# Kernel tuning notes

Measured on AMD Instinct MI355X. Metric: run time of the kernel, lower is better.

## Reference

```python
import jax, jax.numpy as jnp
import numpy as np

NEG_SLOPE = 0.2  # PyG GATConv default negative_slope
EPS = 1e-16      # PyG softmax denominator epsilon


def gat_conv(x, src, dst, W, b, att_src, att_dst, num_nodes):
    """PyG GATConv, heads=1, add_self_loops=True (self loops already in src/dst).
    x: [N, Fin]; src/dst: [E]; W: [Fin, Fout]; att_src/att_dst: [Fout]."""
    h = x @ W                                  # [N, Fout]
    a_src = h @ att_src                        # [N]
    a_dst = h @ att_dst                        # [N]
    e = jax.nn.leaky_relu(a_src[src] + a_dst[dst], NEG_SLOPE)  # [E]
    m = jax.ops.segment_max(e, dst, num_segments=num_nodes)    # softmax over edges grouped by dst
    ex = jnp.exp(e - m[dst])
    denom = jax.ops.segment_sum(ex, dst, num_segments=num_nodes)
    alpha = ex / (denom[dst] + EPS)            # [E]
    out = jax.ops.segment_sum(alpha[:, None] * h[src], dst, num_segments=num_nodes)
    return out + b


def global_attention(x, gate_w, gate_b):
    """PyG GlobalAttention with a single graph: softmax(gate_nn(x)) weighted sum."""
    gate = x @ gate_w + gate_b                 # [N, 1]
    attn = jax.nn.softmax(gate, axis=0)        # softmax over all nodes (one graph)
    return jnp.sum(attn * x, axis=0, keepdims=True)  # [1, F]


def setup_inputs() -> dict:
    key = jax.random.key(0)
    ks = jax.random.split(key, 12)
    N, E, D, H = 50000, 800000, 768, 256
    x = jax.random.normal(ks[0], (N, D), dtype=jnp.float32)
    edge_index = jax.random.randint(ks[1], (2, E), 0, N, dtype=jnp.int64)
    s = 1.0 / np.sqrt(D)
    W1 = jax.random.normal(ks[2], (D, H), dtype=jnp.float32) * s
    b1 = jnp.zeros((H,), dtype=jnp.float32)
    as1 = jax.random.normal(ks[3], (H,), dtype=jnp.float32) * (1.0 / np.sqrt(H))
    ad1 = jax.random.normal(ks[4], (H,), dtype=jnp.float32) * (1.0 / np.sqrt(H))
    s2 = 1.0 / np.sqrt(H)
    W2 = jax.random.normal(ks[5], (H, H), dtype=jnp.float32) * s2
    b2 = jnp.zeros((H,), dtype=jnp.float32)
    as2 = jax.random.normal(ks[6], (H,), dtype=jnp.float32) * s2
    ad2 = jax.random.normal(ks[7], (H,), dtype=jnp.float32) * s2
    gate_w = jax.random.normal(ks[8], (H, 1), dtype=jnp.float32) * s2
    gate_b = jnp.zeros((1,), dtype=jnp.float32)
    return {"x": x, "edge_index": edge_index, "W1": W1, "b1": b1, "as1": as1,
            "ad1": ad1, "W2": W2, "b2": b2, "as2": as2, "ad2": ad2,
            "gate_w": gate_w, "gate_b": gate_b}


def reference(x, edge_index, W1, b1, as1, ad1, W2, b2, as2, ad2, gate_w, gate_b):
    N = x.shape[0]
    loops = jnp.arange(N, dtype=edge_index.dtype)
    src = jnp.concatenate([edge_index[0], loops])  # add self loops (GATConv default)
    dst = jnp.concatenate([edge_index[1], loops])
    h = gat_conv(x, src, dst, W1, b1, as1, ad1, N)
    h = jax.nn.relu(h)
    h = gat_conv(h, src, dst, W2, b2, as2, ad2, N)
    h = jax.nn.relu(h)
    return global_attention(h, gate_w, gate_b)   # [1, 256]
```

## Files before the change

kernel.cpp:

```cpp
#include <hip/hip_runtime.h>

#define WAVE 64
#define LRELU(x) ((x) > 0.0f ? (x) : 0.2f * (x))
#define SB0 __builtin_amdgcn_sched_barrier(0)

typedef __attribute__((ext_vector_type(8))) short bf16x8;
typedef __attribute__((ext_vector_type(8))) unsigned short u16x8;
typedef __attribute__((ext_vector_type(4))) float f32x4;

__device__ __forceinline__ void gld16(const void* g, void* l) {
    __builtin_amdgcn_global_load_lds((const __attribute__((address_space(1))) unsigned int*)g,
                                     (__attribute__((address_space(3))) unsigned int*)l,
                                     16, 0, 0);
}

__device__ __forceinline__ unsigned short f2bf_hi(float f) {
    unsigned u = __builtin_bit_cast(unsigned, f);
    u += 0x7FFF + ((u >> 16) & 1);
    return (unsigned short)(u >> 16);
}

__device__ __forceinline__ void split8(f32x4 a, f32x4 b, bf16x8& hi, bf16x8& lo) {
    float f[8] = {a[0], a[1], a[2], a[3], b[0], b[1], b[2], b[3]};
#pragma unroll
    for (int e = 0; e < 8; e++) {
        unsigned u = __builtin_bit_cast(unsigned, f[e]);
        float hf = __builtin_bit_cast(float, u & 0xFFFF0000u);
        float fl = f[e] - hf;
        unsigned u2 = __builtin_bit_cast(unsigned, fl);
        unsigned t2 = u2 + 0x7FFF + ((u2 >> 16) & 1);
        hi[e] = (short)(u >> 16);
        lo[e] = (short)(t2 >> 16);
    }
}

__device__ __forceinline__ void split8t(f32x4 a, f32x4 b, bf16x8& hi, bf16x8& lo) {
    float f[8] = {a[0], a[1], a[2], a[3], b[0], b[1], b[2], b[3]};
#pragma unroll
    for (int e = 0; e < 8; e++) {
        unsigned u = __builtin_bit_cast(unsigned, f[e]);
        float hf = __builtin_bit_cast(float, u & 0xFFFF0000u);
        float fl = f[e] - hf;
        unsigned u2 = __builtin_bit_cast(unsigned, fl);
        hi[e] = (short)(u >> 16);
        lo[e] = (short)(u2 >> 16);
    }
}

__global__ __launch_bounds__(256) void k_gemm_f32A(const float* __restrict__ A,
                                                   const unsigned short* __restrict__ Bh,
                                                   unsigned short* __restrict__ Cb,
                                                   float* __restrict__ asrc,
                                                   float* __restrict__ adst,
                                                   const float* __restrict__ att_s,
                                                   const float* __restrict__ att_d,
                                                   int M, int K) {
    __shared__ char smem[65536];
    char* bA = smem;
    char* bB = smem + 49152;

    const int tid = threadIdx.x, lane = tid & 63, w = tid >> 6;
    const int m16 = lane & 15, q = lane >> 4;
    const int row0 = blockIdx.x * 128, col0 = blockIdx.y * 128;
    const int NT = K >> 5;

    f32x4 acc[4][4];
#pragma unroll
    for (int i = 0; i < 4; i++)
#pragma unroll
        for (int j = 0; j < 4; j++) acc[i][j] = (f32x4){0.f, 0.f, 0.f, 0.f};

    const float* apt[4];
    const int jA0 = w * 4;
#pragma unroll
    for (int jj = 0; jj < 4; jj++) {
        int j = jA0 + jj;
        int r = row0 + (j & 1) * 64 + lane;
        if (r > M - 1) r = M - 1;
        apt[jj] = A + (size_t)r * K + (j >> 1) * 4;
    }
    const unsigned short* bpt[2];
    const int jB0 = w * 2;
#pragma unroll
    for (int jj = 0; jj < 2; jj++) {
        int j = jB0 + jj;
        bpt[jj] = Bh + (size_t)(col0 + (j & 1) * 64 + lane) * K + (j >> 1) * 8;
    }

    auto stageA = [&](int t, int buf) {
#pragma unroll
        for (int jj = 0; jj < 4; jj++)
            gld16(apt[jj] + (size_t)t * 32, bA + buf * 16384 + (jA0 + jj) * 1024);
    };
    auto stageB = [&](int t, int buf) {
#pragma unroll
        for (int jj = 0; jj < 2; jj++)
            gld16(bpt[jj] + (size_t)t * 32, bB + buf * 8192 + (jB0 + jj) * 1024);
    };

    stageB(0, 0); SB0;
    stageA(0, 0); SB0;
    stageA(1, 1); SB0;
    asm volatile("s_waitcnt vmcnt(4)" ::: "memory");
    __builtin_amdgcn_s_barrier();

    for (int t = 0; t < NT; ++t) {
        if (t + 1 < NT) stageB(t + 1, (t + 1) & 1);
        SB0;
        if (t + 2 < NT) stageA(t + 2, (t + 2) % 3);
        SB0;

        const char* A_ = bA + (t % 3) * 16384;
        const char* B_ = bB + (t & 1) * 8192;
        bf16x8 bh[4];
#pragma unroll
        for (int nt = 0; nt < 4; nt++) {
            int r = (w & 1) * 64 + nt * 16 + m16;
            bh[nt] = *(const bf16x8*)(B_ + q * 2048 + r * 16);
        }
#pragma unroll
        for (int mt = 0; mt < 4; mt++) {
            int r = (w >> 1) * 64 + mt * 16 + m16;
            f32x4 a0 = *(const f32x4*)(A_ + (2 * q) * 2048 + r * 16);
            f32x4 a1 = *(const f32x4*)(A_ + (2 * q + 1) * 2048 + r * 16);
            bf16x8 ah, al;
            split8t(a0, a1, ah, al);
#pragma unroll
            for (int nt = 0; nt < 4; nt++) {
                acc[mt][nt] = __builtin_amdgcn_mfma_f32_16x16x32_bf16(ah, bh[nt], acc[mt][nt], 0, 0, 0);
                acc[mt][nt] = __builtin_amdgcn_mfma_f32_16x16x32_bf16(al, bh[nt], acc[mt][nt], 0, 0, 0);
            }
        }
        SB0;
        if (t + 2 < NT) asm volatile("s_waitcnt vmcnt(4)" ::: "memory");
        else            asm volatile("s_waitcnt vmcnt(0)" ::: "memory");
        __builtin_amdgcn_s_barrier();
    }

    const int rbase = row0 + (w >> 1) * 64;
    const int cbase = col0 + (w & 1) * 64;
#pragma unroll
    for (int mt = 0; mt < 4; mt++)
#pragma unroll
        for (int r = 0; r < 4; r++) {
            int row = rbase + mt * 16 + q * 4 + r;
            if (row < M) {
#pragma unroll
                for (int nt = 0; nt < 4; nt++)
                    Cb[(size_t)row * 256 + cbase + nt * 16 + m16] = f2bf_hi(acc[mt][nt][r]);
            }
        }
    float as_v[4], ad_v[4];
#pragma unroll
    for (int nt = 0; nt < 4; nt++) {
        as_v[nt] = att_s[cbase + nt * 16 + m16];
        ad_v[nt] = att_d[cbase + nt * 16 + m16];
    }
#pragma unroll
    for (int mt = 0; mt < 4; mt++)
#pragma unroll
        for (int r = 0; r < 4; r++) {
            float s = 0.f, d = 0.f;
#pragma unroll
            for (int nt = 0; nt < 4; nt++) {
                float v = acc[mt][nt][r];
                s = fmaf(v, as_v[nt], s);
                d = fmaf(v, ad_v[nt], d);
            }
#pragma unroll
            for (int off = 1; off < 16; off <<= 1) {
                s += __shfl_xor(s, off);
                d += __shfl_xor(d, off);
            }
            int row = rbase + mt * 16 + q * 4 + r;
            if (m16 == 0 && row < M) {
                atomicAdd(&asrc[row], s);
                atomicAdd(&adst[row], d);
            }
        }
}

__global__ __launch_bounds__(256) void k_gemm_bf16A(const unsigned short* __restrict__ Ah,
                                                    const unsigned short* __restrict__ Al,
                                                    const unsigned short* __restrict__ Bh,
                                                    unsigned short* __restrict__ Cb,
                                                    float* __restrict__ asrc,
                                                    float* __restrict__ adst,
                                                    const float* __restrict__ att_s,
                                                    const float* __restrict__ att_d,
                                                    int M, int K) {
    __shared__ char smem[65536];
    char* bAh = smem;
    char* bAl = smem + 24576;
    char* bB  = smem + 49152;

    const int tid = threadIdx.x, lane = tid & 63, w = tid >> 6;
    const int m16 = lane & 15, q = lane >> 4;
    const int row0 = blockIdx.x * 128, col0 = blockIdx.y * 128;
    const int NT = K >> 5;

    f32x4 acc[4][4];
#pragma unroll
    for (int i = 0; i < 4; i++)
#pragma unroll
        for (int j = 0; j < 4; j++) acc[i][j] = (f32x4){0.f, 0.f, 0.f, 0.f};

    const unsigned short* ahpt[2];
    const unsigned short* alpt[2];
    const unsigned short* bpt[2];
    const int j0 = w * 2;
#pragma unroll
    for (int jj = 0; jj < 2; jj++) {
        int j = j0 + jj;
        int ar = row0 + (j & 1) * 64 + lane;
        int br = col0 + (j & 1) * 64 + lane;
        ahpt[jj] = Ah + (size_t)ar * K + (j >> 1) * 8;
        alpt[jj] = Al + (size_t)ar * K + (j >> 1) * 8;
        bpt[jj]  = Bh + (size_t)br * K + (j >> 1) * 8;
    }

    auto stageA = [&](int t, int buf) {
#pragma unroll
        for (int jj = 0; jj < 2; jj++)
            gld16(ahpt[jj] + (size_t)t * 32, bAh + buf * 8192 + (j0 + jj) * 1024);
#pragma unroll
        for (int jj = 0; jj < 2; jj++)
            gld16(alpt[jj] + (size_t)t * 32, bAl + buf * 8192 + (j0 + jj) * 1024);
    };
    auto stageB = [&](int t, int buf) {
#pragma unroll
        for (int jj = 0; jj < 2; jj++)
            gld16(bpt[jj] + (size_t)t * 32, bB + buf * 8192 + (j0 + jj) * 1024);
    };

    stageB(0, 0); SB0;
    stageA(0, 0); SB0;
    stageA(1, 1); SB0;
    asm volatile("s_waitcnt vmcnt(4)" ::: "memory");
    __builtin_amdgcn_s_barrier();

    for (int t = 0; t < NT; ++t) {
        if (t + 1 < NT) stageB(t + 1, (t + 1) & 1);
        SB0;
        if (t + 2 < NT) stageA(t + 2, (t + 2) % 3);
        SB0;

        const char* Ah_ = bAh + (t % 3) * 8192;
        const char* Al_ = bAl + (t % 3) * 8192;
        const char* B_  = bB  + (t & 1) * 8192;
        bf16x8 bh[4];
#pragma unroll
        for (int nt = 0; nt < 4; nt++) {
            int r = (w & 1) * 64 + nt * 16 + m16;
            bh[nt] = *(const bf16x8*)(B_ + q * 2048 + r * 16);
        }
#pragma unroll
        for (int mt = 0; mt < 4; mt++) {
            int r = (w >> 1) * 64 + mt * 16 + m16;
            bf16x8 ah = *(const bf16x8*)(Ah_ + q * 2048 + r * 16);
            bf16x8 al = *(const bf16x8*)(Al_ + q * 2048 + r * 16);
#pragma unroll
            for (int nt = 0; nt < 4; nt++) {
                acc[mt][nt] = __builtin_amdgcn_mfma_f32_16x16x32_bf16(ah, bh[nt], acc[mt][nt], 0, 0, 0);
                acc[mt][nt] = __builtin_amdgcn_mfma_f32_16x16x32_bf16(al, bh[nt], acc[mt][nt], 0, 0, 0);
            }
        }
        SB0;
        if (t + 2 < NT) asm volatile("s_waitcnt vmcnt(4)" ::: "memory");
        else            asm volatile("s_waitcnt vmcnt(0)" ::: "memory");
        __builtin_amdgcn_s_barrier();
    }

    const int rbase = row0 + (w >> 1) * 64;
    const int cbase = col0 + (w & 1) * 64;
#pragma unroll
    for (int mt = 0; mt < 4; mt++)
#pragma unroll
        for (int r = 0; r < 4; r++) {
            int row = rbase + mt * 16 + q * 4 + r;
            if (row < M) {
#pragma unroll
                for (int nt = 0; nt < 4; nt++)
                    Cb[(size_t)row * 256 + cbase + nt * 16 + m16] = f2bf_hi(acc[mt][nt][r]);
            }
        }
    float as_v[4], ad_v[4];
#pragma unroll
    for (int nt = 0; nt < 4; nt++) {
        as_v[nt] = att_s[cbase + nt * 16 + m16];
        ad_v[nt] = att_d[cbase + nt * 16 + m16];
    }
#pragma unroll
    for (int mt = 0; mt < 4; mt++)
#pragma unroll
        for (int r = 0; r < 4; r++) {
            float s = 0.f, d = 0.f;
#pragma unroll
            for (int nt = 0; nt < 4; nt++) {
                float v = acc[mt][nt][r];
                s = fmaf(v, as_v[nt], s);
                d = fmaf(v, ad_v[nt], d);
            }
#pragma unroll
            for (int off = 1; off < 16; off <<= 1) {
                s += __shfl_xor(s, off);
                d += __shfl_xor(d, off);
            }
            int row = rbase + mt * 16 + q * 4 + r;
            if (m16 == 0 && row < M) {
                atomicAdd(&asrc[row], s);
                atomicAdd(&adst[row], d);
            }
        }
}

__global__ __launch_bounds__(256) void k_convB(const float* __restrict__ W,
                                               unsigned short* __restrict__ BThi, int K) {
    int idx = blockIdx.x * 256 + threadIdx.x;
    int k = idx >> 8, n = idx & 255;
    if (k >= K) return;
    BThi[(size_t)n * K + k] = f2bf_hi(W[(size_t)k * 256 + n]);
}

__global__ __launch_bounds__(256) void k_degree(const int* __restrict__ dst,
                                                int* __restrict__ counts, int E) {
    int e = blockIdx.x * 256 + threadIdx.x;
    if (e < E) atomicAdd(&counts[dst[e]], 1);
}

__global__ __launch_bounds__(256) void k_part(const int* __restrict__ counts,
                                              int* __restrict__ psum, int N) {
    __shared__ int red[256];
    int tid = threadIdx.x;
    int i = blockIdx.x * 256 + tid;
    red[tid] = (i < N) ? counts[i] : 0;
    __syncthreads();
    for (int off = 128; off; off >>= 1) {
        if (tid < off) red[tid] += red[tid + off];
        __syncthreads();
    }
    if (tid == 0) psum[blockIdx.x] = red[0];
}

__global__ __launch_bounds__(256) void k_scan_part(int* __restrict__ psum, int nb,
                                                   int* __restrict__ total_out) {
    __shared__ int s[256];
    int tid = threadIdx.x;
    int v = (tid < nb) ? psum[tid] : 0;
    s[tid] = v;
    __syncthreads();
    for (int off = 1; off < 256; off <<= 1) {
        int t = (tid >= off) ? s[tid - off] : 0;
        __syncthreads();
        s[tid] += t;
        __syncthreads();
    }
    if (tid < nb) psum[tid] = s[tid] - v;
    if (tid == 255) *total_out = s[255];
}

__global__ __launch_bounds__(256) void k_rowptr(const int* __restrict__ counts,
                                                const int* __restrict__ psum,
                                                int* __restrict__ rowptr,
                                                int* __restrict__ cursor, int N) {
    __shared__ int s[256];
    int tid = threadIdx.x;
    int i = blockIdx.x * 256 + tid;
    int v = (i < N) ? counts[i] : 0;
    s[tid] = v;
    __syncthreads();
    for (int off = 1; off < 256; off <<= 1) {
        int t = (tid >= off) ? s[tid - off] : 0;
        __syncthreads();
        s[tid] += t;
        __syncthreads();
    }
    if (i < N) {
        int excl = psum[blockIdx.x] + s[tid] - v;
        rowptr[i] = excl;
        cursor[i] = excl;
    }
}

__global__ __launch_bounds__(256) void k_scatter(const int* __restrict__ src,
                                                 const int* __restrict__ dst,
                                                 int* __restrict__ cursor,
                                                 int* __restrict__ col, int E) {
    int e = blockIdx.x * 256 + threadIdx.x;
    if (e < E) {
        int p = atomicAdd(&cursor[dst[e]], 1);
        col[p] = src[e];
    }
}

__global__ __launch_bounds__(256) void k_edge(const unsigned short* __restrict__ hb,
                                              const float* __restrict__ asrc,
                                              const float* __restrict__ adst,
                                              const float* __restrict__ gmaxv,
                                              const int* __restrict__ rowptr,
                                              const int* __restrict__ col,
                                              const float* __restrict__ bias,
                                              float* __restrict__ outf,
                                              unsigned short* __restrict__ outh,
                                              unsigned short* __restrict__ outl,
                                              const float* __restrict__ gw,
                                              const float* __restrict__ gb,
                                              float* __restrict__ gatep, int N) {
    int hw = threadIdx.x >> 5;
    int l  = threadIdx.x & 31;
    int node = blockIdx.x * 8 + hw;
    if (node >= N) return;
    int j = rowptr[node], end = rowptr[node + 1];
    float ad = adst[node];
    float m = LRELU(gmaxv[0] + ad);

    float a[8];
    float wself = __expf(LRELU(asrc[node] + ad) - m);
    u16x8 hv = *(const u16x8*)&hb[(size_t)node * 256 + l * 8];
#pragma unroll
    for (int e = 0; e < 8; e++)
        a[e] = wself * __builtin_bit_cast(float, (unsigned)hv[e] << 16);
    float denom = wself;

    for (; j + 4 <= end; j += 4) {
        int s0 = col[j], s1 = col[j + 1], s2 = col[j + 2], s3 = col[j + 3];
        float w0 = __expf(LRELU(asrc[s0] + ad) - m);
        float w1 = __expf(LRELU(asrc[s1] + ad) - m);
        float w2 = __expf(LRELU(asrc[s2] + ad) - m);
        float w3 = __expf(LRELU(asrc[s3] + ad) - m);
        denom += w0 + w1 + w2 + w3;
        u16x8 h0 = *(const u16x8*)&hb[(size_t)s0 * 256 + l * 8];
        u16x8 h1 = *(const u16x8*)&hb[(size_t)s1 * 256 + l * 8];
        u16x8 h2 = *(const u16x8*)&hb[(size_t)s2 * 256 + l * 8];
        u16x8 h3 = *(const u16x8*)&hb[(size_t)s3 * 256 + l * 8];
#pragma unroll
        for (int e = 0; e < 8; e++) {
            float f0 = __builtin_bit_cast(float, (unsigned)h0[e] << 16);
            float f1 = __builtin_bit_cast(float, (unsigned)h1[e] << 16);
            float f2 = __builtin_bit_cast(float, (unsigned)h2[e] << 16);
            float f3 = __builtin_bit_cast(float, (unsigned)h3[e] << 16);
            a[e] = fmaf(w0, f0, fmaf(w1, f1, fmaf(w2, f2, fmaf(w3, f3, a[e]))));
        }
    }
    for (; j < end; j++) {
        int s = col[j];
        float wgt = __expf(LRELU(asrc[s] + ad) - m);
        denom += wgt;
        u16x8 hx = *(const u16x8*)&hb[(size_t)s * 256 + l * 8];
#pragma unroll
        for (int e = 0; e < 8; e++)
            a[e] = fmaf(wgt, __builtin_bit_cast(float, (unsigned)hx[e] << 16), a[e]);
    }
    float inv = 1.0f / (denom + 1e-16f);
#pragma unroll
    for (int e = 0; e < 8; e++) a[e] *= inv;

    float o[8];
    {
        float4 bv0 = *(const float4*)&bias[l * 8];
        float4 bv1 = *(const float4*)&bias[l * 8 + 4];
        float bb[8] = {bv0.x, bv0.y, bv0.z, bv0.w, bv1.x, bv1.y, bv1.z, bv1.w};
#pragma unroll
        for (int e = 0; e < 8; e++) o[e] = fmaxf(a[e] + bb[e], 0.0f);
    }
    if (outf) {
        float4 o0 = make_float4(o[0], o[1], o[2], o[3]);
        float4 o1 = make_float4(o[4], o[5], o[6], o[7]);
        *(float4*)&outf[(size_t)node * 256 + l * 8]     = o0;
        *(float4*)&outf[(size_t)node * 256 + l * 8 + 4] = o1;
    }
    if (outh) {
        u16x8 ph, pl;
#pragma unroll
        for (int e = 0; e < 8; e++) {
            unsigned u = __builtin_bit_cast(unsigned, o[e]);
            float hf = __builtin_bit_cast(float, u & 0xFFFF0000u);
            float fl = o[e] - hf;
            unsigned u2 = __builtin_bit_cast(unsigned, fl);
            unsigned t2 = u2 + 0x7FFF + ((u2 >> 16) & 1);
            ph[e] = (unsigned short)(u >> 16);
            pl[e] = (unsigned short)(t2 >> 16);
        }
        *(u16x8*)&outh[(size_t)node * 256 + l * 8] = ph;
        *(u16x8*)&outl[(size_t)node * 256 + l * 8] = pl;
    }
    if (gatep) {
        float s = 0.f;
#pragma unroll
        for (int e = 0; e < 8; e++) s = fmaf(o[e], gw[l * 8 + e], s);
#pragma unroll
        for (int off = 16; off; off >>= 1) s += __shfl_xor(s, off);
        if (l == 0) gatep[node] = s + gb[0];
    }
}

__global__ __launch_bounds__(256) void k_pmax(const float* __restrict__ v, int N,
                                              float* __restrict__ pmax) {
    __shared__ float red[256];
    int tid = threadIdx.x;
    float m = -3.0e38f;
    for (int i = blockIdx.x * 256 + tid; i < N; i += gridDim.x * 256) m = fmaxf(m, v[i]);
    red[tid] = m;
    __syncthreads();
    for (int off = 128; off; off >>= 1) {
        if (tid < off) red[tid] = fmaxf(red[tid], red[tid + off]);
        __syncthreads();
    }
    if (tid == 0) pmax[blockIdx.x] = red[0];
}

__global__ __launch_bounds__(64) void k_fold(const float* __restrict__ p,
                                             float* __restrict__ o) {
    int lane = threadIdx.x;
    float m = p[lane];
#pragma unroll
    for (int off = 32; off; off >>= 1) m = fmaxf(m, __shfl_xor(m, off));
    if (lane == 0) o[0] = m;
}

__global__ __launch_bounds__(256) void k_gmid(const float* __restrict__ pmax, int nb,
                                              float* __restrict__ scal,
                                              float* __restrict__ gout) {
    __shared__ float red[256];
    int tid = threadIdx.x;
    red[tid] = (tid < nb) ? pmax[tid] : -3.0e38f;
    __syncthreads();
    for (int off = 128; off; off >>= 1) {
        if (tid < off) red[tid] = fmaxf(red[tid], red[tid + off]);
        __syncthreads();
    }
    if (tid == 0) { scal[0] = red[0]; scal[1] = 0.0f; }
    gout[tid] = 0.0f;
}

__global__ __launch_bounds__(256) void k_gout(const float* __restrict__ h,
                                              const float* __restrict__ gate,
                                              float* __restrict__ scal_rw,
                                              float* __restrict__ gout, int N) {
    int f = threadIdx.x;
    float gmax = scal_rw[0];
    float acc = 0.0f, sumw = 0.0f;
    for (int i = blockIdx.x; i < N; i += gridDim.x) {
        float w = __expf(gate[i] - gmax);
        acc = fmaf(w, h[(size_t)i * 256 + f], acc);
        sumw += w;
    }
    atomicAdd(&gout[f], acc);
    if (f == 0) atomicAdd(&scal_rw[1], sumw);
}

__global__ __launch_bounds__(256) void k_final(const float* __restrict__ gout,
                                               const float* __restrict__ scal,
                                               float* __restrict__ out) {
    int f = threadIdx.x;
    out[f] = gout[f] / scal[1];
}

extern "C" void kernel_launch(void* const* d_in, const int* in_sizes, int n_in,
                              void* d_out, int out_size, void* d_ws, size_t ws_size,
                              hipStream_t stream) {
    const float* x   = (const float*)d_in[0];
    const int*   ei  = (const int*)d_in[1];
    const float* W1  = (const float*)d_in[2];
    const float* b1  = (const float*)d_in[3];
    const float* as1 = (const float*)d_in[4];
    const float* ad1 = (const float*)d_in[5];
    const float* W2  = (const float*)d_in[6];
    const float* b2  = (const float*)d_in[7];
    const float* as2 = (const float*)d_in[8];
    const float* ad2 = (const float*)d_in[9];
    const float* gw  = (const float*)d_in[10];
    const float* gb  = (const float*)d_in[11];
    float* out = (float*)d_out;

    const int N = in_sizes[0] / 768;
    const int E = in_sizes[1] / 2;
    const int Mpad = (N + 127) & ~127;
    const int* srcA = ei;
    const int* dstA = ei + E;

    char* w = (char*)d_ws;
    auto alloc = [&](size_t bytes) -> void* {
        void* p = (void*)w;
        w += (bytes + 255) & ~(size_t)255;
        return p;
    };
    unsigned short* bufHb = (unsigned short*)alloc((size_t)N * 256 * 2);
    unsigned short* X2h = (unsigned short*)alloc((size_t)Mpad * 256 * 2);
    unsigned short* X2l = (unsigned short*)alloc((size_t)Mpad * 256 * 2);
    float* bufX = (float*)X2h;
    float* asrc   = (float*)alloc((size_t)N * 4);
    float* adst   = (float*)alloc((size_t)N * 4);
    float* gate   = (float*)alloc((size_t)N * 4);
    int*   counts = (int*)alloc((size_t)N * 4);
    int*   rowptr = (int*)alloc((size_t)(N + 1) * 4);
    int*   cursor = (int*)alloc((size_t)N * 4);
    int*   colbuf = (int*)alloc((size_t)E * 4);
    int*   psum   = (int*)alloc(256 * 4);
    float* pmax   = (float*)alloc(256 * 4);
    float* gmaxv  = (float*)alloc(4 * 4);
    float* scal   = (float*)alloc(8 * 4);
    float* gout   = (float*)alloc(256 * 4);
    unsigned short* BT1 = (unsigned short*)alloc((size_t)256 * 768 * 2);
    unsigned short* BT2 = (unsigned short*)alloc((size_t)256 * 256 * 2);

    const int eb  = (E + 255) / 256;
    const int nb8 = (N + 7) / 8;
    const int nb  = (N + 255) / 256;
    const dim3 gg(Mpad / 128, 2);

    k_convB<<<768, 256, 0, stream>>>(W1, BT1, 768);
    k_convB<<<256, 256, 0, stream>>>(W2, BT2, 256);

    (void)hipMemsetAsync(counts, 0, (size_t)N * 4, stream);
    k_degree<<<eb, 256, 0, stream>>>(dstA, counts, E);
    k_part<<<nb, 256, 0, stream>>>(counts, psum, N);
    k_scan_part<<<1, 256, 0, stream>>>(psum, nb, rowptr + N);
    k_rowptr<<<nb, 256, 0, stream>>>(counts, psum, rowptr, cursor, N);
    k_scatter<<<eb, 256, 0, stream>>>(srcA, dstA, cursor, colbuf, E);

    (void)hipMemsetAsync(asrc, 0, (size_t)N * 4, stream);
    (void)hipMemsetAsync(adst, 0, (size_t)N * 4, stream);
    k_gemm_f32A<<<gg, 256, 0, stream>>>(x, BT1, bufHb, asrc, adst, as1, ad1, N, 768);
    k_pmax<<<64, 256, 0, stream>>>(asrc, N, pmax);
    k_fold<<<1, 64, 0, stream>>>(pmax, gmaxv);
    k_edge<<<nb8, 256, 0, stream>>>(bufHb, asrc, adst, gmaxv, rowptr, colbuf, b1,
                                    nullptr, X2h, X2l, nullptr, nullptr, nullptr, N);

    (void)hipMemsetAsync(asrc, 0, (size_t)N * 4, stream);
    (void)hipMemsetAsync(adst, 0, (size_t)N * 4, stream);
    k_gemm_bf16A<<<gg, 256, 0, stream>>>(X2h, X2l, BT2, bufHb, asrc, adst, as2, ad2, N, 256);
    k_pmax<<<64, 256, 0, stream>>>(asrc, N, pmax);
    k_fold<<<1, 64, 0, stream>>>(pmax, gmaxv);
    k_edge<<<nb8, 256, 0, stream>>>(bufHb, asrc, adst, gmaxv, rowptr, colbuf, b2,
                                    bufX, nullptr, nullptr, gw, gb, gate, N);

    k_pmax<<<64, 256, 0, stream>>>(gate, N, pmax);
    k_gmid<<<1, 256, 0, stream>>>(pmax, 64, scal, gout);
    k_gout<<<256, 256, 0, stream>>>(bufX, gate, scal, gout, N);
    k_final<<<1, 256, 0, stream>>>(gout, scal, out);
}
```

Baseline: 630.1 us.

## Use XOR-swizzled row-major LDS tiles with double buffering in both GEMMs

Both GEMM kernels now load A and B tiles row-major into LDS, applying an XOR swizzle on the 16-byte chunk index so that global loads are row-contiguous and the LDS reads used by the MFMA fragments avoid bank conflicts. The A pipeline is reduced from triple to double buffering, which cuts LDS from 64KB to 48KB per block and may allow more resident blocks per CU. In exchange, the loop now waits for all outstanding loads (vmcnt(0)) every iteration, so there is less prefetch depth to hide global memory latency.

```diff
diff --git a/kernel.cpp b/kernel.cpp
--- a/kernel.cpp
+++ b/kernel.cpp
@@ -55,9 +55,9 @@
                                                    const float* __restrict__ att_s,
                                                    const float* __restrict__ att_d,
                                                    int M, int K) {
-    __shared__ char smem[65536];
+    __shared__ char smem[49152];
     char* bA = smem;
-    char* bB = smem + 49152;
+    char* bB = smem + 32768;
 
     const int tid = threadIdx.x, lane = tid & 63, w = tid >> 6;
     const int m16 = lane & 15, q = lane >> 4;
@@ -75,16 +75,20 @@
 #pragma unroll
     for (int jj = 0; jj < 4; jj++) {
         int j = jA0 + jj;
-        int r = row0 + (j & 1) * 64 + lane;
-        if (r > M - 1) r = M - 1;
-        apt[jj] = A + (size_t)r * K + (j >> 1) * 4;
+        int r = j * 8 + (lane >> 3);
+        int grow = row0 + r;
+        if (grow > M - 1) grow = M - 1;
+        int s = (lane & 7) ^ ((lane >> 3) & 7);
+        apt[jj] = A + (size_t)grow * K + s * 4;
     }
     const unsigned short* bpt[2];
     const int jB0 = w * 2;
 #pragma unroll
     for (int jj = 0; jj < 2; jj++) {
         int j = jB0 + jj;
-        bpt[jj] = Bh + (size_t)(col0 + (j & 1) * 64 + lane) * K + (j >> 1) * 8;
+        int r = j * 16 + (lane >> 2);
+        int s = (lane & 3) ^ ((lane >> 3) & 3);
+        bpt[jj] = Bh + (size_t)(col0 + r) * K + s * 8;
     }
 
     auto stageA = [&](int t, int buf) {
@@ -100,29 +104,32 @@
 
     stageB(0, 0); SB0;
     stageA(0, 0); SB0;
-    stageA(1, 1); SB0;
-    asm volatile("s_waitcnt vmcnt(4)" ::: "memory");
+    asm volatile("s_waitcnt vmcnt(0)" ::: "memory");
     __builtin_amdgcn_s_barrier();
 
     for (int t = 0; t < NT; ++t) {
-        if (t + 1 < NT) stageB(t + 1, (t + 1) & 1);
+        if (t + 1 < NT) {
+            stageB(t + 1, (t + 1) & 1);
+            stageA(t + 1, (t + 1) & 1);
+        }
         SB0;
-        if (t + 2 < NT) stageA(t + 2, (t + 2) % 3);
-        SB0;
-
-        const char* A_ = bA + (t % 3) * 16384;
+
+        const char* A_ = bA + (t & 1) * 16384;
         const char* B_ = bB + (t & 1) * 8192;
         bf16x8 bh[4];
 #pragma unroll
         for (int nt = 0; nt < 4; nt++) {
             int r = (w & 1) * 64 + nt * 16 + m16;
-            bh[nt] = *(const bf16x8*)(B_ + q * 2048 + r * 16);
+            int p = q ^ ((r >> 1) & 3);
+            bh[nt] = *(const bf16x8*)(B_ + r * 64 + p * 16);
         }
 #pragma unroll
         for (int mt = 0; mt < 4; mt++) {
             int r = (w >> 1) * 64 + mt * 16 + m16;
-            f32x4 a0 = *(const f32x4*)(A_ + (2 * q) * 2048 + r * 16);
-            f32x4 a1 = *(const f32x4*)(A_ + (2 * q + 1) * 2048 + r * 16);
+            int p0 = (2 * q) ^ (r & 7);
+            int p1 = (2 * q + 1) ^ (r & 7);
+            f32x4 a0 = *(const f32x4*)(A_ + r * 128 + p0 * 16);
+            f32x4 a1 = *(const f32x4*)(A_ + r * 128 + p1 * 16);
             bf16x8 ah, al;
             split8t(a0, a1, ah, al);
 #pragma unroll
@@ -132,8 +139,7 @@
             }
         }
         SB0;
-        if (t + 2 < NT) asm volatile("s_waitcnt vmcnt(4)" ::: "memory");
-        else            asm volatile("s_waitcnt vmcnt(0)" ::: "memory");
+        asm volatile("s_waitcnt vmcnt(0)" ::: "memory");
         __builtin_amdgcn_s_barrier();
     }
 
@@ -189,10 +195,10 @@
                                                     const float* __restrict__ att_s,
                                                     const float* __restrict__ att_d,
                                                     int M, int K) {
-    __shared__ char smem[65536];
+    __shared__ char smem[49152];
     char* bAh = smem;
-    char* bAl = smem + 24576;
-    char* bB  = smem + 49152;
+    char* bAl = smem + 16384;
+    char* bB  = smem + 32768;
 
     const int tid = threadIdx.x, lane = tid & 63, w = tid >> 6;
     const int m16 = lane & 15, q = lane >> 4;
@@ -212,14 +218,17 @@
 #pragma unroll
     for (int jj = 0; jj < 2; jj++) {
         int j = j0 + jj;
-        int ar = row0 + (j & 1) * 64 + lane;
-        int br = col0 + (j & 1) * 64 + lane;
-        ahpt[jj] = Ah + (size_t)ar * K + (j >> 1) * 8;
-        alpt[jj] = Al + (size_t)ar * K + (j >> 1) * 8;
-        bpt[jj]  = Bh + (size_t)br * K + (j >> 1) * 8;
-    }
-
-    auto stageA = [&](int t, int buf) {
+        int r = j * 16 + (lane >> 2);
+        int s = (lane & 3) ^ ((lane >> 3) & 3);
+        ahpt[jj] = Ah + (size_t)(row0 + r) * K + s * 8;
+        alpt[jj] = Al + (size_t)(row0 + r) * K + s * 8;
+        bpt[jj]  = Bh + (size_t)(col0 + r) * K + s * 8;
+    }
+
+    auto stageAll = [&](int t, int buf) {
+#pragma unroll
+        for (int jj = 0; jj < 2; jj++)
+            gld16(bpt[jj] + (size_t)t * 32, bB + buf * 8192 + (j0 + jj) * 1024);
 #pragma unroll
         for (int jj = 0; jj < 2; jj++)
             gld16(ahpt[jj] + (size_t)t * 32, bAh + buf * 8192 + (j0 + jj) * 1024);
@@ -227,38 +236,31 @@
         for (int jj = 0; jj < 2; jj++)
             gld16(alpt[jj] + (size_t)t * 32, bAl + buf * 8192 + (j0 + jj) * 1024);
     };
-    auto stageB = [&](int t, int buf) {
-#pragma unroll
-        for (int jj = 0; jj < 2; jj++)
-            gld16(bpt[jj] + (size_t)t * 32, bB + buf * 8192 + (j0 + jj) * 1024);
-    };
-
-    stageB(0, 0); SB0;
-    stageA(0, 0); SB0;
-    stageA(1, 1); SB0;
-    asm volatile("s_waitcnt vmcnt(4)" ::: "memory");
+
+    stageAll(0, 0); SB0;
+    asm volatile("s_waitcnt vmcnt(0)" ::: "memory");
     __builtin_amdgcn_s_barrier();
 
     for (int t = 0; t < NT; ++t) {
-        if (t + 1 < NT) stageB(t + 1, (t + 1) & 1);
+        if (t + 1 < NT) stageAll(t + 1, (t + 1) & 1);
         SB0;
-        if (t + 2 < NT) stageA(t + 2, (t + 2) % 3);
-        SB0;
-
-        const char* Ah_ = bAh + (t % 3) * 8192;
-        const char* Al_ = bAl + (t % 3) * 8192;
+
+        const char* Ah_ = bAh + (t & 1) * 8192;
+        const char* Al_ = bAl + (t & 1) * 8192;
         const char* B_  = bB  + (t & 1) * 8192;
         bf16x8 bh[4];
 #pragma unroll
         for (int nt = 0; nt < 4; nt++) {
             int r = (w & 1) * 64 + nt * 16 + m16;
-            bh[nt] = *(const bf16x8*)(B_ + q * 2048 + r * 16);
+            int p = q ^ ((r >> 1) & 3);
+            bh[nt] = *(const bf16x8*)(B_ + r * 64 + p * 16);
         }
 #pragma unroll
         for (int mt = 0; mt < 4; mt++) {
             int r = (w >> 1) * 64 + mt * 16 + m16;
-            bf16x8 ah = *(const bf16x8*)(Ah_ + q * 2048 + r * 16);
-            bf16x8 al = *(const bf16x8*)(Al_ + q * 2048 + r * 16);
+            int p = q ^ ((r >> 1) & 3);
+            bf16x8 ah = *(const bf16x8*)(Ah_ + r * 64 + p * 16);
+            bf16x8 al = *(const bf16x8*)(Al_ + r * 64 + p * 16);
 #pragma unroll
             for (int nt = 0; nt < 4; nt++) {
                 acc[mt][nt] = __builtin_amdgcn_mfma_f32_16x16x32_bf16(ah, bh[nt], acc[mt][nt], 0, 0, 0);
@@ -266,8 +268,7 @@
             }
         }
         SB0;
-        if (t + 2 < NT) asm volatile("s_waitcnt vmcnt(4)" ::: "memory");
-        else            asm volatile("s_waitcnt vmcnt(0)" ::: "memory");
+        asm volatile("s_waitcnt vmcnt(0)" ::: "memory");
         __builtin_amdgcn_s_barrier();
     }
 
```

After: 599.4 us. -4.9%, faster.
